# Optimization experiments

Measured on AMD Instinct MI355X. Metric: run time of the kernel, lower is better.

## Reference

```python
import jax, jax.numpy as jnp
import numpy as np

B, S, FC, FO = 16, 512, 24, 16
D, H, DK, FF, L = 512, 8, 64, 2048, 4
MAXPOS = 512
EPS = 1e-6


def _ln(x, scale, bias):
    mu = jnp.mean(x, axis=-1, keepdims=True)
    var = jnp.mean((x - mu) ** 2, axis=-1, keepdims=True)
    return (x - mu) * jax.lax.rsqrt(var + EPS) * scale + bias


def setup_inputs() -> dict:
    key = jax.random.key(0)
    ks = iter(jax.random.split(key, 64))
    def rn(shape, s=0.02):
        return (jax.random.normal(next(ks), shape, dtype=jnp.float32) * s)
    inp = {
        'x_cgm': jax.random.normal(next(ks), (B, S, FC), dtype=jnp.float32),
        'x_other': jax.random.normal(next(ks), (B, FO), dtype=jnp.float32),
        'cgm_W': rn((FC, D)), 'cgm_b': jnp.zeros((D,), jnp.float32),
        'rel_emb': rn((2 * MAXPOS - 1, DK)),
        'Wq': rn((L, D, H * DK)), 'bq': jnp.zeros((L, H * DK), jnp.float32),
        'Wk': rn((L, D, H * DK)), 'bk': jnp.zeros((L, H * DK), jnp.float32),
        'Wv': rn((L, D, H * DK)), 'bv': jnp.zeros((L, H * DK), jnp.float32),
        'Wo': rn((L, H * DK, D)), 'bo': jnp.zeros((L, D), jnp.float32),
        'Wg': rn((L, D, D)), 'bg': jnp.zeros((L, D), jnp.float32),
        'Wf1': rn((L, D, FF)), 'bf1': jnp.zeros((L, FF), jnp.float32),
        'Wfg': rn((L, D, FF)), 'bfg': jnp.zeros((L, FF), jnp.float32),
        'Wf2': rn((L, FF, D)), 'bf2': jnp.zeros((L, D), jnp.float32),
        'ln1_s': jnp.ones((L, D), jnp.float32), 'ln1_b': jnp.zeros((L, D), jnp.float32),
        'ln2_s': jnp.ones((L, D), jnp.float32), 'ln2_b': jnp.zeros((L, D), jnp.float32),
        'other_W': rn((FO, D)), 'other_b': jnp.zeros((D,), jnp.float32),
        'fW1': rn((2 * D, 256)), 'fb1': jnp.zeros((256,), jnp.float32),
        'fln1_s': jnp.ones((256,), jnp.float32), 'fln1_b': jnp.zeros((256,), jnp.float32),
        'fW2': rn((256, 128)), 'fb2': jnp.zeros((128,), jnp.float32),
        'fln2_s': jnp.ones((128,), jnp.float32), 'fln2_b': jnp.zeros((128,), jnp.float32),
        'fW3': rn((128, 1)), 'fb3': jnp.zeros((1,), jnp.float32),
    }
    return inp


def reference(x_cgm, x_other, cgm_W, cgm_b, rel_emb, Wq, bq, Wk, bk, Wv, bv,
              Wo, bo, Wg, bg, Wf1, bf1, Wfg, bfg, Wf2, bf2,
              ln1_s, ln1_b, ln2_s, ln2_b, other_W, other_b,
              fW1, fb1, fln1_s, fln1_b, fW2, fb2, fln2_s, fln2_b, fW3, fb3):
    x = x_cgm @ cgm_W + cgm_b  # [B,S,D]
    # relative position bias: rel_emb[i-j+MAXPOS-1] -> [S,S,DK], reduced by mean over depth
    idx = jnp.arange(S)
    pos_idx = idx[:, None] - idx[None, :] + MAXPOS - 1
    pos_bias = jnp.mean(rel_emb[pos_idx], axis=-1)  # [S,S]
    scale = jnp.sqrt(jnp.float32(DK))
    for l in range(L):
        q = (x @ Wq[l] + bq[l]).reshape(B, S, H, DK)
        k = (x @ Wk[l] + bk[l]).reshape(B, S, H, DK)
        v = (x @ Wv[l] + bv[l]).reshape(B, S, H, DK)
        scores = jnp.einsum('bqhd,bkhd->bhqk', q, k) / scale + pos_bias  # [B,H,S,S]
        probs = jax.nn.softmax(scores, axis=-1)
        ctx = jnp.einsum('bhqk,bkhd->bqhd', probs, v).reshape(B, S, H * DK)
        att = ctx @ Wo[l] + bo[l]
        gate = jax.nn.sigmoid(x @ Wg[l] + bg[l])
        x = _ln(x + gate * att, ln1_s[l], ln1_b[l])
        ff = (x @ Wf1[l] + bf1[l]) * jax.nn.sigmoid(x @ Wfg[l] + bfg[l])
        ff = ff @ Wf2[l] + bf2[l]
        x = _ln(x + ff, ln2_s[l], ln2_b[l])
    x = jnp.mean(x, axis=1)  # [B,D]
    xo = x_other @ other_W + other_b
    h = jnp.concatenate([x, xo], axis=-1)  # [B,2D]
    h = jax.nn.relu(_ln(h @ fW1 + fb1, fln1_s, fln1_b))
    h = jax.nn.relu(_ln(h @ fW2 + fb2, fln2_s, fln2_b))
    return h @ fW3 + fb3  # [B,1]
```

## Files before the change

kernel.cpp:

```cpp
#include <hip/hip_runtime.h>
#include <math.h>

constexpr int Bn = 16;
constexpr int Sn = 512;
constexpr int FCn = 24;
constexpr int FOn = 16;
constexpr int Dn = 512;
constexpr int Hn = 8;
constexpr int DKn = 64;
constexpr int FFn = 2048;
constexpr int Ln = 4;
constexpr int MAXPOSn = 512;
constexpr float EPSf = 1e-6f;

typedef __attribute__((ext_vector_type(8))) short bf16x8;
typedef __attribute__((ext_vector_type(4))) float floatx4;

__device__ __forceinline__ float sigmoidf_(float x) { return 1.0f / (1.0f + __expf(-x)); }

__device__ __forceinline__ unsigned short f2bf(float f) {
  unsigned int u = __float_as_uint(f);
  u += 0x7fffu + ((u >> 16) & 1u);
  return (unsigned short)(u >> 16);
}
__device__ __forceinline__ float b2f(unsigned short b) {
  return __uint_as_float(((unsigned int)b) << 16);
}

__device__ __forceinline__ void g2l16(const void* g, void* l) {
  __builtin_amdgcn_global_load_lds((const __attribute__((address_space(1))) void*)g,
                                   (__attribute__((address_space(3))) void*)l, 16, 0, 0);
}

__device__ __forceinline__ void st_bf16_pair(unsigned short* dst, float v, int lane) {
  unsigned int us = f2bf(v);
  unsigned int other = (unsigned int)__shfl_xor((int)us, 1);
  if (!(lane & 1)) *(unsigned int*)dst = us | (other << 16);
}

__device__ __forceinline__ float waveReduceSum(float v) {
  #pragma unroll
  for (int off = 32; off >= 1; off >>= 1) v += __shfl_xor(v, off);
  return v;
}

__device__ __forceinline__ float blockReduceSum(float v) {
  v = waveReduceSum(v);
  __shared__ float red[8];
  const int w = threadIdx.x >> 6;
  const int nw = blockDim.x >> 6;
  if ((threadIdx.x & 63) == 0) red[w] = v;
  __syncthreads();
  float r = 0.0f;
  for (int i = 0; i < nw; ++i) r += red[i];
  __syncthreads();
  return r;
}

__global__ __launch_bounds__(256) void wconv_kernel(
    const float* __restrict__ in, unsigned short* __restrict__ out,
    int K, int N, size_t inStride, size_t outStride) {
  __shared__ float tile[32][33];
  in += (size_t)blockIdx.z * inStride;
  out += (size_t)blockIdx.z * outStride;
  const int k0 = blockIdx.y * 32, n0 = blockIdx.x * 32;
  const int tr = threadIdx.x >> 3;
  const int tc4 = (threadIdx.x & 7) * 4;
  float4 vv = *(const float4*)&in[(size_t)(k0 + tr) * N + n0 + tc4];
  tile[tr][tc4 + 0] = vv.x; tile[tr][tc4 + 1] = vv.y;
  tile[tr][tc4 + 2] = vv.z; tile[tr][tc4 + 3] = vv.w;
  __syncthreads();
  ushort4 o4;
  o4.x = f2bf(tile[tc4 + 0][tr]); o4.y = f2bf(tile[tc4 + 1][tr]);
  o4.z = f2bf(tile[tc4 + 2][tr]); o4.w = f2bf(tile[tc4 + 3][tr]);
  *(ushort4*)&out[(size_t)(n0 + tr) * K + k0 + tc4] = o4;
}

__global__ void bcat_kernel(const float* __restrict__ bq, const float* __restrict__ bk,
                            const float* __restrict__ bv, const float* __restrict__ bg,
                            float* __restrict__ out) {
  const int t = blockIdx.x * 256 + threadIdx.x;
  const int l = t >> 11;
  const int c = t & 2047;
  float v;
  if (c < 512) v = bq[l * 512 + c];
  else if (c < 1024) v = bk[l * 512 + c - 512];
  else if (c < 1536) v = bv[l * 512 + c - 1024];
  else v = bg[l * 512 + c - 1536];
  out[t] = v;
}

__global__ __launch_bounds__(256) void embed_kernel(
    const float* __restrict__ xc, const float* __restrict__ W,
    const float* __restrict__ bias, float* __restrict__ x,
    unsigned short* __restrict__ xb) {
  const int idx = blockIdx.x * 256 + threadIdx.x;
  const int n = idx & (Dn - 1);
  const int m = idx >> 9;
  const float* xr = xc + m * FCn;
  float acc = bias[n];
  #pragma unroll
  for (int k = 0; k < FCn; ++k) acc = fmaf(xr[k], W[k * Dn + n], acc);
  x[idx] = acc;
  xb[idx] = f2bf(acc);
}

__global__ void relmean_kernel(const float* __restrict__ rel, float* __restrict__ rm) {
  const int p = blockIdx.x * blockDim.x + threadIdx.x;
  if (p >= 2 * MAXPOSn - 1) return;
  float s = 0.0f;
  #pragma unroll 8
  for (int d = 0; d < DKn; ++d) s += rel[p * DKn + d];
  rm[p] = s * (1.0f / DKn);
}

template <int EPI>
__global__ __launch_bounds__(256) void mgemm(
    const unsigned short* __restrict__ A, const unsigned short* __restrict__ Bt,
    const float* __restrict__ bias, float* __restrict__ Cf,
    unsigned short* __restrict__ Cb, unsigned short* __restrict__ Cb2,
    int Astride, int N, int Koff, int Klen, int ldc, int nt) {
  __shared__ unsigned short As[128 * 64];
  __shared__ unsigned short Bs[128 * 64];
  const int t = threadIdx.x;
  const int w = t >> 6;
  const int lane = t & 63;
  const int id = blockIdx.x;
  const int xcd = id & 7;
  const int lid = id >> 3;
  const int n0 = (lid % nt) * 128;
  const int m0 = (xcd * 8 + lid / nt) * 128;
  const int wm = (w >> 1) * 64;
  const int wn = (w & 1) * 64;
  const int lr = lane & 15;
  const int lq = lane >> 4;

  floatx4 acc[4][4];
  #pragma unroll
  for (int i = 0; i < 4; ++i)
    #pragma unroll
    for (int j = 0; j < 4; ++j) acc[i][j] = (floatx4){0.f, 0.f, 0.f, 0.f};

  const int srow = lane >> 3;
  const int sg = ((lane & 7) ^ srow) * 8;
  const int r7 = lr & 7;
  const int p0 = (lq ^ r7) * 8;
  const int p1 = ((4 + lq) ^ r7) * 8;

  for (int k0 = Koff; k0 < Koff + Klen; k0 += 64) {
    __syncthreads();
    #pragma unroll
    for (int r = 0; r < 4; ++r) {
      const int rb = (w * 4 + r) * 8;
      g2l16(&A[(size_t)(m0 + rb + srow) * Astride + k0 + sg], &As[rb * 64]);
      g2l16(&Bt[(size_t)(n0 + rb + srow) * Astride + k0 + sg], &Bs[rb * 64]);
    }
    __syncthreads();
    #pragma unroll
    for (int s = 0; s < 2; ++s) {
      const int ps = s ? p1 : p0;
      bf16x8 af[4], bf[4];
      #pragma unroll
      for (int i = 0; i < 4; ++i)
        af[i] = *(const bf16x8*)&As[(wm + i * 16 + lr) * 64 + ps];
      #pragma unroll
      for (int j = 0; j < 4; ++j)
        bf[j] = *(const bf16x8*)&Bs[(wn + j * 16 + lr) * 64 + ps];
      #pragma unroll
      for (int i = 0; i < 4; ++i)
        #pragma unroll
        for (int j = 0; j < 4; ++j)
          acc[i][j] = __builtin_amdgcn_mfma_f32_16x16x32_bf16(af[i], bf[j], acc[i][j], 0, 0, 0);
    }
  }

  #pragma unroll
  for (int i = 0; i < 4; ++i) {
    const int row = m0 + wm + i * 16 + lq * 4;
    #pragma unroll
    for (int j = 0; j < 4; ++j) {
      const int col = n0 + wn + j * 16 + lr;
      const int colp = col & ~1;
      #pragma unroll
      for (int r = 0; r < 4; ++r) {
        if (EPI == 0) {
          Cf[(size_t)(row + r) * ldc + col] = acc[i][j][r] + bias[col];
        } else if (EPI == 5) {
          const size_t idx = (size_t)(row + r) * ldc + col;
          Cf[idx] += acc[i][j][r];
        } else if (EPI == 3) {
          st_bf16_pair(&Cb[(size_t)(row + r) * ldc + colp], acc[i][j][r] + bias[col], lane);
        } else if (EPI == 4) {
          const float va = acc[i][j][r] + bias[col];
          if (col < 1536)
            st_bf16_pair(&Cb[(size_t)(row + r) * 1536 + colp], va, lane);
          else
            st_bf16_pair(&Cb2[(size_t)(row + r) * 512 + (colp - 1536)], sigmoidf_(va), lane);
        }
      }
    }
  }
}

__global__ __launch_bounds__(256) void ffgemm(
    const unsigned short* __restrict__ A, const unsigned short* __restrict__ B1t,
    const unsigned short* __restrict__ B2t, const float* __restrict__ b1,
    const float* __restrict__ b2, unsigned short* __restrict__ C, int K) {
  __shared__ unsigned short As[128 * 64];
  __shared__ unsigned short B1s[64 * 64];
  __shared__ unsigned short B2s[64 * 64];
  const int t = threadIdx.x;
  const int w = t >> 6;
  const int lane = t & 63;
  const int id = blockIdx.x;
  const int xcd = id & 7;
  const int lid = id >> 3;
  const int n0 = (lid & 31) * 64;
  const int m0 = (xcd * 8 + (lid >> 5)) * 128;
  const int wm = (w >> 1) * 64;
  const int wn = (w & 1) * 32;
  const int lr = lane & 15;
  const int lq = lane >> 4;

  floatx4 a1[4][2], a2[4][2];
  #pragma unroll
  for (int i = 0; i < 4; ++i)
    #pragma unroll
    for (int j = 0; j < 2; ++j) {
      a1[i][j] = (floatx4){0.f, 0.f, 0.f, 0.f};
      a2[i][j] = (floatx4){0.f, 0.f, 0.f, 0.f};
    }

  const int srow = lane >> 3;
  const int sg = ((lane & 7) ^ srow) * 8;
  const int r7 = lr & 7;
  const int p0 = (lq ^ r7) * 8;
  const int p1 = ((4 + lq) ^ r7) * 8;

  for (int k0 = 0; k0 < K; k0 += 64) {
    __syncthreads();
    #pragma unroll
    for (int r = 0; r < 4; ++r) {
      const int rb = (w * 4 + r) * 8;
      g2l16(&A[(size_t)(m0 + rb + srow) * K + k0 + sg], &As[rb * 64]);
    }
    #pragma unroll
    for (int r = 0; r < 2; ++r) {
      const int rb = (w * 2 + r) * 8;
      g2l16(&B1t[(size_t)(n0 + rb + srow) * K + k0 + sg], &B1s[rb * 64]);
      g2l16(&B2t[(size_t)(n0 + rb + srow) * K + k0 + sg], &B2s[rb * 64]);
    }
    __syncthreads();
    #pragma unroll
    for (int s = 0; s < 2; ++s) {
      const int ps = s ? p1 : p0;
      bf16x8 af[4], f1[2], f2[2];
      #pragma unroll
      for (int i = 0; i < 4; ++i)
        af[i] = *(const bf16x8*)&As[(wm + i * 16 + lr) * 64 + ps];
      #pragma unroll
      for (int j = 0; j < 2; ++j) {
        f1[j] = *(const bf16x8*)&B1s[(wn + j * 16 + lr) * 64 + ps];
        f2[j] = *(const bf16x8*)&B2s[(wn + j * 16 + lr) * 64 + ps];
      }
      #pragma unroll
      for (int i = 0; i < 4; ++i)
        #pragma unroll
        for (int j = 0; j < 2; ++j) {
          a1[i][j] = __builtin_amdgcn_mfma_f32_16x16x32_bf16(af[i], f1[j], a1[i][j], 0, 0, 0);
          a2[i][j] = __builtin_amdgcn_mfma_f32_16x16x32_bf16(af[i], f2[j], a2[i][j], 0, 0, 0);
        }
    }
  }

  #pragma unroll
  for (int i = 0; i < 4; ++i) {
    const int row = m0 + wm + i * 16 + lq * 4;
    #pragma unroll
    for (int j = 0; j < 2; ++j) {
      const int col = n0 + wn + j * 16 + lr;
      const int colp = col & ~1;
      const float bb1 = b1[col], bb2 = b2[col];
      #pragma unroll
      for (int r = 0; r < 4; ++r) {
        const float f = (a1[i][j][r] + bb1) * sigmoidf_(a2[i][j][r] + bb2);
        st_bf16_pair(&C[(size_t)(row + r) * 2048 + colp], f, lane);
      }
    }
  }
}

__global__ __launch_bounds__(256) void attn_kernel(
    const unsigned short* __restrict__ qkv, const float* __restrict__ rm,
    unsigned short* __restrict__ ctx) {
  __shared__ unsigned short Ks[64 * 72];
  __shared__ unsigned short Vt[64 * 72];
  __shared__ unsigned short Pw[4][16 * 72];
  __shared__ float rml[576];
  const int t = threadIdx.x;
  const int w = t >> 6;
  const int lane = t & 63;
  const int lr = lane & 15;
  const int lq = lane >> 4;
  const int bid = blockIdx.x;
  const int b = bid & 15;
  const int h = (bid >> 4) & 7;
  const int qt = bid >> 7;
  const int q0 = qt * 64;
  const size_t rowb = (size_t)b * Sn * 1536;

  for (int i = t; i < 576; i += 256) rml[i] = rm[q0 + i];

  bf16x8 aq0, aq1;
  {
    const unsigned short* qp = &qkv[rowb + (size_t)(q0 + w * 16 + lr) * 1536 + h * 64 + lq * 8];
    aq0 = *(const bf16x8*)qp;
    aq1 = *(const bf16x8*)(qp + 32);
  }

  floatx4 o_acc[4];
  #pragma unroll
  for (int i = 0; i < 4; ++i) o_acc[i] = (floatx4){0.f, 0.f, 0.f, 0.f};
  float m_old[4] = {-1e30f, -1e30f, -1e30f, -1e30f};
  float l_sum[4] = {0.f, 0.f, 0.f, 0.f};

  const int skey = t >> 2;
  const int schk = (t & 3) * 16;
  const int vkp = t >> 4;
  const int vd4 = (t & 15) * 4;

  for (int kc = 0; kc < 8; ++kc) {
    __syncthreads();
    {
      const unsigned short* gk = &qkv[rowb + (size_t)(kc * 64 + skey) * 1536 + 512 + h * 64 + schk];
      *(bf16x8*)&Ks[skey * 72 + schk] = *(const bf16x8*)gk;
      *(bf16x8*)&Ks[skey * 72 + schk + 8] = *(const bf16x8*)(gk + 8);
    }
    #pragma unroll
    for (int pass = 0; pass < 2; ++pass) {
      const int kp = vkp + pass * 16;
      const unsigned short* gv = &qkv[rowb + (size_t)(kc * 64 + kp * 2) * 1536 + 1024 + h * 64 + vd4];
      ushort4 v0 = *(const ushort4*)gv;
      ushort4 v1 = *(const ushort4*)(gv + 1536);
      *(ushort2*)&Vt[(vd4 + 0) * 72 + kp * 2] = make_ushort2(v0.x, v1.x);
      *(ushort2*)&Vt[(vd4 + 1) * 72 + kp * 2] = make_ushort2(v0.y, v1.y);
      *(ushort2*)&Vt[(vd4 + 2) * 72 + kp * 2] = make_ushort2(v0.z, v1.z);
      *(ushort2*)&Vt[(vd4 + 3) * 72 + kp * 2] = make_ushort2(v0.w, v1.w);
    }
    __syncthreads();

    floatx4 s_acc[4];
    #pragma unroll
    for (int j = 0; j < 4; ++j) {
      bf16x8 b0 = *(const bf16x8*)&Ks[(j * 16 + lr) * 72 + lq * 8];
      bf16x8 b1 = *(const bf16x8*)&Ks[(j * 16 + lr) * 72 + 32 + lq * 8];
      s_acc[j] = __builtin_amdgcn_mfma_f32_16x16x32_bf16(aq0, b0, (floatx4){0.f, 0.f, 0.f, 0.f}, 0, 0, 0);
      s_acc[j] = __builtin_amdgcn_mfma_f32_16x16x32_bf16(aq1, b1, s_acc[j], 0, 0, 0);
    }

    float mloc[4] = {-1e30f, -1e30f, -1e30f, -1e30f};
    #pragma unroll
    for (int j = 0; j < 4; ++j) {
      const int key = kc * 64 + j * 16 + lr;
      #pragma unroll
      for (int r = 0; r < 4; ++r) {
        const float sv = s_acc[j][r] * 0.125f + rml[(w * 16 + lq * 4 + r) + 511 - key];
        s_acc[j][r] = sv;
        mloc[r] = fmaxf(mloc[r], sv);
      }
    }
    #pragma unroll
    for (int off = 1; off <= 8; off <<= 1)
      #pragma unroll
      for (int r = 0; r < 4; ++r) mloc[r] = fmaxf(mloc[r], __shfl_xor(mloc[r], off));

    float alpha[4], rsum[4];
    #pragma unroll
    for (int r = 0; r < 4; ++r) {
      const float mnew = fmaxf(m_old[r], mloc[r]);
      alpha[r] = __expf(m_old[r] - mnew);
      m_old[r] = mnew;
      rsum[r] = 0.f;
    }
    #pragma unroll
    for (int j = 0; j < 4; ++j)
      #pragma unroll
      for (int r = 0; r < 4; ++r) {
        const float p = __expf(s_acc[j][r] - m_old[r]);
        rsum[r] += p;
        Pw[w][(lq * 4 + r) * 72 + j * 16 + lr] = f2bf(p);
      }
    #pragma unroll
    for (int off = 1; off <= 8; off <<= 1)
      #pragma unroll
      for (int r = 0; r < 4; ++r) rsum[r] += __shfl_xor(rsum[r], off);
    #pragma unroll
    for (int r = 0; r < 4; ++r) l_sum[r] = l_sum[r] * alpha[r] + rsum[r];
    #pragma unroll
    for (int i = 0; i < 4; ++i)
      #pragma unroll
      for (int r = 0; r < 4; ++r) o_acc[i][r] *= alpha[r];

    bf16x8 ap0 = *(const bf16x8*)&Pw[w][lr * 72 + lq * 8];
    bf16x8 ap1 = *(const bf16x8*)&Pw[w][lr * 72 + 32 + lq * 8];
    #pragma unroll
    for (int i = 0; i < 4; ++i) {
      bf16x8 v0 = *(const bf16x8*)&Vt[(i * 16 + lr) * 72 + lq * 8];
      bf16x8 v1 = *(const bf16x8*)&Vt[(i * 16 + lr) * 72 + 32 + lq * 8];
      o_acc[i] = __builtin_amdgcn_mfma_f32_16x16x32_bf16(ap0, v0, o_acc[i], 0, 0, 0);
      o_acc[i] = __builtin_amdgcn_mfma_f32_16x16x32_bf16(ap1, v1, o_acc[i], 0, 0, 0);
    }
  }

  float rinv[4];
  #pragma unroll
  for (int r = 0; r < 4; ++r) rinv[r] = 1.0f / l_sum[r];
  #pragma unroll
  for (int i = 0; i < 4; ++i)
    #pragma unroll
    for (int r = 0; r < 4; ++r) {
      const int q = q0 + w * 16 + lq * 4 + r;
      ctx[((size_t)(b * Sn + q)) * Dn + h * 64 + i * 16 + lr] = f2bf(o_acc[i][r] * rinv[r]);
    }
}

__global__ __launch_bounds__(256) void ln_res1_kernel(
    float* __restrict__ x, unsigned short* __restrict__ xb,
    const unsigned short* __restrict__ att, const unsigned short* __restrict__ gate,
    const float* __restrict__ s, const float* __restrict__ bsh) {
  const int w = threadIdx.x >> 6, lane = threadIdx.x & 63;
  const int row = blockIdx.x * 4 + w;
  const size_t base = (size_t)row * Dn;
  const int c = lane * 4;
  float4 xv0 = *(const float4*)&x[base + c];
  float4 xv1 = *(const float4*)&x[base + c + 256];
  ushort4 a0 = *(const ushort4*)&att[base + c];
  ushort4 a1 = *(const ushort4*)&att[base + c + 256];
  ushort4 g0 = *(const ushort4*)&gate[base + c];
  ushort4 g1 = *(const ushort4*)&gate[base + c + 256];
  float y[8];
  y[0] = xv0.x + b2f(a0.x) * b2f(g0.x);
  y[1] = xv0.y + b2f(a0.y) * b2f(g0.y);
  y[2] = xv0.z + b2f(a0.z) * b2f(g0.z);
  y[3] = xv0.w + b2f(a0.w) * b2f(g0.w);
  y[4] = xv1.x + b2f(a1.x) * b2f(g1.x);
  y[5] = xv1.y + b2f(a1.y) * b2f(g1.y);
  y[6] = xv1.z + b2f(a1.z) * b2f(g1.z);
  y[7] = xv1.w + b2f(a1.w) * b2f(g1.w);
  float sum = 0.f;
  #pragma unroll
  for (int i = 0; i < 8; ++i) sum += y[i];
  const float mu = waveReduceSum(sum) * (1.0f / Dn);
  float vs = 0.f;
  #pragma unroll
  for (int i = 0; i < 8; ++i) { y[i] -= mu; vs += y[i] * y[i]; }
  const float rstd = rsqrtf(waveReduceSum(vs) * (1.0f / Dn) + EPSf);
  float4 s0 = *(const float4*)&s[c], s1 = *(const float4*)&s[c + 256];
  float4 b0 = *(const float4*)&bsh[c], b1 = *(const float4*)&bsh[c + 256];
  float4 o0, o1;
  o0.x = y[0] * rstd * s0.x + b0.x; o0.y = y[1] * rstd * s0.y + b0.y;
  o0.z = y[2] * rstd * s0.z + b0.z; o0.w = y[3] * rstd * s0.w + b0.w;
  o1.x = y[4] * rstd * s1.x + b1.x; o1.y = y[5] * rstd * s1.y + b1.y;
  o1.z = y[6] * rstd * s1.z + b1.z; o1.w = y[7] * rstd * s1.w + b1.w;
  *(float4*)&x[base + c] = o0;
  *(float4*)&x[base + c + 256] = o1;
  ushort4 ob0, ob1;
  ob0.x = f2bf(o0.x); ob0.y = f2bf(o0.y); ob0.z = f2bf(o0.z); ob0.w = f2bf(o0.w);
  ob1.x = f2bf(o1.x); ob1.y = f2bf(o1.y); ob1.z = f2bf(o1.z); ob1.w = f2bf(o1.w);
  *(ushort4*)&xb[base + c] = ob0;
  *(ushort4*)&xb[base + c + 256] = ob1;
}

__global__ __launch_bounds__(256) void ln_res2_kernel(
    float* __restrict__ x, unsigned short* __restrict__ xb,
    const float* __restrict__ add, const float* __restrict__ s,
    const float* __restrict__ bsh) {
  const int w = threadIdx.x >> 6, lane = threadIdx.x & 63;
  const int row = blockIdx.x * 4 + w;
  const size_t base = (size_t)row * Dn;
  const int c = lane * 4;
  float4 xv0 = *(const float4*)&x[base + c];
  float4 xv1 = *(const float4*)&x[base + c + 256];
  float4 a0 = *(const float4*)&add[base + c];
  float4 a1 = *(const float4*)&add[base + c + 256];
  float y[8] = {xv0.x + a0.x, xv0.y + a0.y, xv0.z + a0.z, xv0.w + a0.w,
                xv1.x + a1.x, xv1.y + a1.y, xv1.z + a1.z, xv1.w + a1.w};
  float sum = 0.f;
  #pragma unroll
  for (int i = 0; i < 8; ++i) sum += y[i];
  const float mu = waveReduceSum(sum) * (1.0f / Dn);
  float vs = 0.f;
  #pragma unroll
  for (int i = 0; i < 8; ++i) { y[i] -= mu; vs += y[i] * y[i]; }
  const float rstd = rsqrtf(waveReduceSum(vs) * (1.0f / Dn) + EPSf);
  float4 s0 = *(const float4*)&s[c], s1 = *(const float4*)&s[c + 256];
  float4 b0 = *(const float4*)&bsh[c], b1 = *(const float4*)&bsh[c + 256];
  float4 o0, o1;
  o0.x = y[0] * rstd * s0.x + b0.x; o0.y = y[1] * rstd * s0.y + b0.y;
  o0.z = y[2] * rstd * s0.z + b0.z; o0.w = y[3] * rstd * s0.w + b0.w;
  o1.x = y[4] * rstd * s1.x + b1.x; o1.y = y[5] * rstd * s1.y + b1.y;
  o1.z = y[6] * rstd * s1.z + b1.z; o1.w = y[7] * rstd * s1.w + b1.w;
  *(float4*)&x[base + c] = o0;
  *(float4*)&x[base + c + 256] = o1;
  ushort4 ob0, ob1;
  ob0.x = f2bf(o0.x); ob0.y = f2bf(o0.y); ob0.z = f2bf(o0.z); ob0.w = f2bf(o0.w);
  ob1.x = f2bf(o1.x); ob1.y = f2bf(o1.y); ob1.z = f2bf(o1.z); ob1.w = f2bf(o1.w);
  *(ushort4*)&xb[base + c] = ob0;
  *(ushort4*)&xb[base + c + 256] = ob1;
}

__global__ __launch_bounds__(256) void mp_part_kernel(const float* __restrict__ x,
                                                      float* __restrict__ part) {
  const int b = blockIdx.x, sc = blockIdx.y;
  const int t = threadIdx.x;
  float s0 = 0.f, s1 = 0.f;
  for (int si = sc * 64; si < sc * 64 + 64; ++si) {
    s0 += x[((size_t)(b * Sn + si)) * Dn + t];
    s1 += x[((size_t)(b * Sn + si)) * Dn + t + 256];
  }
  part[(size_t)(b * 8 + sc) * 512 + t] = s0;
  part[(size_t)(b * 8 + sc) * 512 + t + 256] = s1;
}

__global__ __launch_bounds__(256) void mp_comb_xo_kernel(
    const float* __restrict__ part, const float* __restrict__ xo,
    const float* __restrict__ oW, const float* __restrict__ ob,
    float* __restrict__ h) {
  const int idx = blockIdx.x * 256 + threadIdx.x;
  const int b = idx >> 9, d = idx & 511;
  float s = 0.f;
  #pragma unroll
  for (int i = 0; i < 8; ++i) s += part[(size_t)(b * 8 + i) * 512 + d];
  h[b * 1024 + d] = s * (1.0f / Sn);
  float acc = ob[d];
  #pragma unroll
  for (int k = 0; k < FOn; ++k) acc = fmaf(xo[b * FOn + k], oW[k * Dn + d], acc);
  h[b * 1024 + 512 + d] = acc;
}

__global__ __launch_bounds__(256) void f1a_kernel(
    const float* __restrict__ h, const float* __restrict__ W,
    float* __restrict__ part) {
  const int b = blockIdx.x, kq = blockIdx.y;
  const int n = threadIdx.x;
  const float* hr = h + b * 1024 + kq * 128;
  const float* Wp = W + (size_t)(kq * 128) * 256 + n;
  float acc = 0.f;
  #pragma unroll 8
  for (int k = 0; k < 128; ++k) acc = fmaf(hr[k], Wp[(size_t)k * 256], acc);
  part[(size_t)(b * 8 + kq) * 256 + n] = acc;
}

__global__ __launch_bounds__(256) void tail_kernel(
    const float* __restrict__ part, const float* __restrict__ fb1,
    const float* __restrict__ fln1_s, const float* __restrict__ fln1_b,
    const float* __restrict__ fW2, const float* __restrict__ fb2,
    const float* __restrict__ fln2_s, const float* __restrict__ fln2_b,
    const float* __restrict__ fW3, const float* __restrict__ fb3,
    float* __restrict__ out) {
  __shared__ float h1[256];
  const int b = blockIdx.x;
  const int t = threadIdx.x;
  float acc = fb1[t];
  #pragma unroll
  for (int i = 0; i < 8; ++i) acc += part[(size_t)(b * 8 + i) * 256 + t];
  float mu = blockReduceSum(acc) * (1.0f / 256.0f);
  float d = acc - mu;
  float var = blockReduceSum(d * d) * (1.0f / 256.0f);
  h1[t] = fmaxf(d * rsqrtf(var + EPSf) * fln1_s[t] + fln1_b[t], 0.0f);
  __syncthreads();
  float acc2 = 0.f;
  if (t < 128) {
    #pragma unroll 8
    for (int k = 0; k < 256; ++k) acc2 = fmaf(h1[k], fW2[k * 128 + t], acc2);
    acc2 += fb2[t];
  }
  mu = blockReduceSum(t < 128 ? acc2 : 0.f) * (1.0f / 128.0f);
  d = (t < 128) ? acc2 - mu : 0.f;
  var = blockReduceSum(d * d) * (1.0f / 128.0f);
  float v = 0.f;
  if (t < 128) {
    const float h2v = fmaxf(d * rsqrtf(var + EPSf) * fln2_s[t] + fln2_b[t], 0.0f);
    v = h2v * fW3[t];
  }
  v = blockReduceSum(v);
  if (t == 0) out[b] = v + fb3[0];
}

extern "C" void kernel_launch(void* const* d_in, const int* in_sizes, int n_in,
                              void* d_out, int out_size, void* d_ws, size_t ws_size,
                              hipStream_t stream) {
  (void)in_sizes; (void)n_in; (void)out_size; (void)ws_size;
  const float* x_cgm  = (const float*)d_in[0];
  const float* x_other= (const float*)d_in[1];
  const float* cgm_W  = (const float*)d_in[2];
  const float* cgm_b  = (const float*)d_in[3];
  const float* rel_emb= (const float*)d_in[4];
  const float* Wq = (const float*)d_in[5];
  const float* bq = (const float*)d_in[6];
  const float* Wk = (const float*)d_in[7];
  const float* bk = (const float*)d_in[8];
  const float* Wv = (const float*)d_in[9];
  const float* bv = (const float*)d_in[10];
  const float* Wo = (const float*)d_in[11];
  const float* bo = (const float*)d_in[12];
  const float* Wg = (const float*)d_in[13];
  const float* bg = (const float*)d_in[14];
  const float* Wf1 = (const float*)d_in[15];
  const float* bf1 = (const float*)d_in[16];
  const float* Wfg = (const float*)d_in[17];
  const float* bfg = (const float*)d_in[18];
  const float* Wf2 = (const float*)d_in[19];
  const float* bf2 = (const float*)d_in[20];
  const float* ln1_s = (const float*)d_in[21];
  const float* ln1_b = (const float*)d_in[22];
  const float* ln2_s = (const float*)d_in[23];
  const float* ln2_b = (const float*)d_in[24];
  const float* other_W = (const float*)d_in[25];
  const float* other_b = (const float*)d_in[26];
  const float* fW1 = (const float*)d_in[27];
  const float* fb1 = (const float*)d_in[28];
  const float* fln1_s = (const float*)d_in[29];
  const float* fln1_b = (const float*)d_in[30];
  const float* fW2 = (const float*)d_in[31];
  const float* fb2 = (const float*)d_in[32];
  const float* fln2_s = (const float*)d_in[33];
  const float* fln2_b = (const float*)d_in[34];
  const float* fW3 = (const float*)d_in[35];
  const float* fb3 = (const float*)d_in[36];
  float* out = (float*)d_out;

  char* p = (char*)d_ws;
  auto alloc = [&](size_t bytes) { char* r = p; p += (bytes + 255) & ~(size_t)255; return r; };
  float*          X      = (float*)alloc((size_t)8192 * 512 * 4);
  unsigned short* Xb     = (unsigned short*)alloc((size_t)8192 * 512 * 2);
  unsigned short* QKVb   = (unsigned short*)alloc((size_t)8192 * 1536 * 2);
  unsigned short* CTXb   = (unsigned short*)alloc((size_t)8192 * 512 * 2);
  char*           R      = alloc((size_t)8192 * 2048 * 2);
  unsigned short* ATTb   = (unsigned short*)R;
  unsigned short* GATEb  = (unsigned short*)(R + (size_t)8192 * 512 * 2);
  unsigned short* FFBh   = (unsigned short*)R;
  float*          CTXo   = (float*)QKVb;
  unsigned short* Wqkvgt = (unsigned short*)alloc((size_t)4 * 2048 * 512 * 2);
  unsigned short* Wot    = (unsigned short*)alloc((size_t)4 * 512 * 512 * 2);
  unsigned short* Wf1t   = (unsigned short*)alloc((size_t)4 * 2048 * 512 * 2);
  unsigned short* Wfgt   = (unsigned short*)alloc((size_t)4 * 2048 * 512 * 2);
  unsigned short* Wf2t   = (unsigned short*)alloc((size_t)4 * 512 * 2048 * 2);
  float*          bqkvg  = (float*)alloc((size_t)4 * 2048 * 4);
  float*          RMb    = (float*)alloc(1024 * 4);
  float*          Hb     = (float*)alloc(16 * 1024 * 4);
  float*          MPP    = (float*)alloc((size_t)16 * 8 * 512 * 4);
  float*          F1P    = (float*)alloc((size_t)16 * 8 * 256 * 4);

  wconv_kernel<<<dim3(16, 16, 4), 256, 0, stream>>>(Wq, Wqkvgt + (size_t)0 * 512, 512, 512,
                                                    (size_t)512 * 512, (size_t)2048 * 512);
  wconv_kernel<<<dim3(16, 16, 4), 256, 0, stream>>>(Wk, Wqkvgt + (size_t)512 * 512, 512, 512,
                                                    (size_t)512 * 512, (size_t)2048 * 512);
  wconv_kernel<<<dim3(16, 16, 4), 256, 0, stream>>>(Wv, Wqkvgt + (size_t)1024 * 512, 512, 512,
                                                    (size_t)512 * 512, (size_t)2048 * 512);
  wconv_kernel<<<dim3(16, 16, 4), 256, 0, stream>>>(Wg, Wqkvgt + (size_t)1536 * 512, 512, 512,
                                                    (size_t)512 * 512, (size_t)2048 * 512);
  wconv_kernel<<<dim3(16, 16, 4), 256, 0, stream>>>(Wo, Wot, 512, 512,
                                                    (size_t)512 * 512, (size_t)512 * 512);
  wconv_kernel<<<dim3(64, 16, 4), 256, 0, stream>>>(Wf1, Wf1t, 512, 2048,
                                                    (size_t)512 * 2048, (size_t)2048 * 512);
  wconv_kernel<<<dim3(64, 16, 4), 256, 0, stream>>>(Wfg, Wfgt, 512, 2048,
                                                    (size_t)512 * 2048, (size_t)2048 * 512);
  wconv_kernel<<<dim3(16, 64, 4), 256, 0, stream>>>(Wf2, Wf2t, 2048, 512,
                                                    (size_t)2048 * 512, (size_t)512 * 2048);
  bcat_kernel<<<dim3(32), 256, 0, stream>>>(bq, bk, bv, bg, bqkvg);

  embed_kernel<<<dim3(16384), dim3(256), 0, stream>>>(x_cgm, cgm_W, cgm_b, X, Xb);
  relmean_kernel<<<dim3(4), dim3(256), 0, stream>>>(rel_emb, RMb);

  for (int l = 0; l < Ln; ++l) {
    const size_t bof = (size_t)l * Dn;
    mgemm<4><<<dim3(1024), 256, 0, stream>>>(Xb, Wqkvgt + (size_t)l * 2048 * 512,
                                             bqkvg + (size_t)l * 2048, nullptr, QKVb, GATEb,
                                             512, 2048, 0, 512, 0, 16);
    attn_kernel<<<dim3(1024), dim3(256), 0, stream>>>(QKVb, RMb, CTXb);
    mgemm<3><<<dim3(256), 256, 0, stream>>>(CTXb, Wot + (size_t)l * 512 * 512,
                                            bo + bof, nullptr, ATTb, nullptr,
                                            512, 512, 0, 512, 512, 4);
    ln_res1_kernel<<<dim3(2048), 256, 0, stream>>>(X, Xb, ATTb, GATEb, ln1_s + bof, ln1_b + bof);
    ffgemm<<<dim3(2048), 256, 0, stream>>>(Xb, Wf1t + (size_t)l * 2048 * 512,
                                           Wfgt + (size_t)l * 2048 * 512,
                                           bf1 + (size_t)l * FFn, bfg + (size_t)l * FFn,
                                           FFBh, 512);
    mgemm<0><<<dim3(256), 256, 0, stream>>>(FFBh, Wf2t + (size_t)l * 512 * 2048,
                                            bf2 + bof, CTXo, nullptr, nullptr,
                                            2048, 512, 0, 1024, 512, 4);
    mgemm<5><<<dim3(256), 256, 0, stream>>>(FFBh, Wf2t + (size_t)l * 512 * 2048,
                                            nullptr, CTXo, nullptr, nullptr,
                                            2048, 512, 1024, 1024, 512, 4);
    ln_res2_kernel<<<dim3(2048), 256, 0, stream>>>(X, Xb, CTXo, ln2_s + bof, ln2_b + bof);
  }

  mp_part_kernel<<<dim3(16, 8), 256, 0, stream>>>(X, MPP);
  mp_comb_xo_kernel<<<dim3(32), 256, 0, stream>>>(MPP, x_other, other_W, other_b, Hb);
  f1a_kernel<<<dim3(16, 8), 256, 0, stream>>>(Hb, fW1, F1P);
  tail_kernel<<<dim3(16), 256, 0, stream>>>(F1P, fb1, fln1_s, fln1_b,
                                            fW2, fb2, fln2_s, fln2_b, fW3, fb3, out);
}
```

Baseline: 1.213 ms.

## Shrink GEMM K-tile to 32, add 128x64 GEMM for N=512, drop split-K

All bf16 MFMA GEMMs now stage K tiles of 32 instead of 64, with a plain unswizzled LDS layout and one MFMA step per tile. A new mgemm_n64 kernel with 128x64 output tiles handles the two N=512 GEMMs (output projection and FF down-projection) on 512 blocks instead of 256. The FF down-projection is no longer split into two K halves accumulated through a read-modify-write pass; one kernel covers the full K=2048. The aim is more parallelism, less LDS per block and one fewer launch, at the cost of twice as many barriers per K, possible LDS bank conflicts without the XOR swizzle, and less reuse per tile.

Result: faster. 1.101 ms (-9.2%).

```diff
diff --git a/kernel.cpp b/kernel.cpp
--- a/kernel.cpp
+++ b/kernel.cpp
@@ -119,9 +119,9 @@
     const unsigned short* __restrict__ A, const unsigned short* __restrict__ Bt,
     const float* __restrict__ bias, float* __restrict__ Cf,
     unsigned short* __restrict__ Cb, unsigned short* __restrict__ Cb2,
-    int Astride, int N, int Koff, int Klen, int ldc, int nt) {
-  __shared__ unsigned short As[128 * 64];
-  __shared__ unsigned short Bs[128 * 64];
+    int Astride, int N, int Klen, int ldc, int nt) {
+  __shared__ unsigned short As[128 * 32];
+  __shared__ unsigned short Bs[128 * 32];
   const int t = threadIdx.x;
   const int w = t >> 6;
   const int lane = t & 63;
@@ -141,37 +141,30 @@
     #pragma unroll
     for (int j = 0; j < 4; ++j) acc[i][j] = (floatx4){0.f, 0.f, 0.f, 0.f};
 
-  const int srow = lane >> 3;
-  const int sg = ((lane & 7) ^ srow) * 8;
-  const int r7 = lr & 7;
-  const int p0 = (lq ^ r7) * 8;
-  const int p1 = ((4 + lq) ^ r7) * 8;
-
-  for (int k0 = Koff; k0 < Koff + Klen; k0 += 64) {
+  const int srow = lane >> 2;
+  const int schk = (lane & 3) * 8;
+
+  for (int k0 = 0; k0 < Klen; k0 += 32) {
     __syncthreads();
     #pragma unroll
-    for (int r = 0; r < 4; ++r) {
-      const int rb = (w * 4 + r) * 8;
-      g2l16(&A[(size_t)(m0 + rb + srow) * Astride + k0 + sg], &As[rb * 64]);
-      g2l16(&Bt[(size_t)(n0 + rb + srow) * Astride + k0 + sg], &Bs[rb * 64]);
+    for (int r = 0; r < 2; ++r) {
+      const int rb = (w * 2 + r) * 16;
+      g2l16(&A[(size_t)(m0 + rb + srow) * Astride + k0 + schk], &As[rb * 32]);
+      g2l16(&Bt[(size_t)(n0 + rb + srow) * Astride + k0 + schk], &Bs[rb * 32]);
     }
     __syncthreads();
-    #pragma unroll
-    for (int s = 0; s < 2; ++s) {
-      const int ps = s ? p1 : p0;
-      bf16x8 af[4], bf[4];
-      #pragma unroll
-      for (int i = 0; i < 4; ++i)
-        af[i] = *(const bf16x8*)&As[(wm + i * 16 + lr) * 64 + ps];
+    bf16x8 af[4], bf[4];
+    #pragma unroll
+    for (int i = 0; i < 4; ++i)
+      af[i] = *(const bf16x8*)&As[(wm + i * 16 + lr) * 32 + lq * 8];
+    #pragma unroll
+    for (int j = 0; j < 4; ++j)
+      bf[j] = *(const bf16x8*)&Bs[(wn + j * 16 + lr) * 32 + lq * 8];
+    #pragma unroll
+    for (int i = 0; i < 4; ++i)
       #pragma unroll
       for (int j = 0; j < 4; ++j)
-        bf[j] = *(const bf16x8*)&Bs[(wn + j * 16 + lr) * 64 + ps];
-      #pragma unroll
-      for (int i = 0; i < 4; ++i)
-        #pragma unroll
-        for (int j = 0; j < 4; ++j)
-          acc[i][j] = __builtin_amdgcn_mfma_f32_16x16x32_bf16(af[i], bf[j], acc[i][j], 0, 0, 0);
-    }
+        acc[i][j] = __builtin_amdgcn_mfma_f32_16x16x32_bf16(af[i], bf[j], acc[i][j], 0, 0, 0);
   }
 
   #pragma unroll
@@ -185,9 +178,6 @@
       for (int r = 0; r < 4; ++r) {
         if (EPI == 0) {
           Cf[(size_t)(row + r) * ldc + col] = acc[i][j][r] + bias[col];
-        } else if (EPI == 5) {
-          const size_t idx = (size_t)(row + r) * ldc + col;
-          Cf[idx] += acc[i][j][r];
         } else if (EPI == 3) {
           st_bf16_pair(&Cb[(size_t)(row + r) * ldc + colp], acc[i][j][r] + bias[col], lane);
         } else if (EPI == 4) {
@@ -202,13 +192,85 @@
   }
 }
 
+template <int EPI>
+__global__ __launch_bounds__(256) void mgemm_n64(
+    const unsigned short* __restrict__ A, const unsigned short* __restrict__ Bt,
+    const float* __restrict__ bias, float* __restrict__ Cf,
+    unsigned short* __restrict__ Cb, int Astride, int Klen, int ldc) {
+  __shared__ unsigned short As[128 * 32];
+  __shared__ unsigned short Bs[64 * 32];
+  const int t = threadIdx.x;
+  const int w = t >> 6;
+  const int lane = t & 63;
+  const int id = blockIdx.x;
+  const int xcd = id & 7;
+  const int lid = id >> 3;
+  const int n0 = (lid & 7) * 64;
+  const int m0 = (xcd * 8 + (lid >> 3)) * 128;
+  const int wm = (w >> 1) * 64;
+  const int wn = (w & 1) * 32;
+  const int lr = lane & 15;
+  const int lq = lane >> 4;
+
+  floatx4 acc[4][2];
+  #pragma unroll
+  for (int i = 0; i < 4; ++i)
+    #pragma unroll
+    for (int j = 0; j < 2; ++j) acc[i][j] = (floatx4){0.f, 0.f, 0.f, 0.f};
+
+  const int srow = lane >> 2;
+  const int schk = (lane & 3) * 8;
+
+  for (int k0 = 0; k0 < Klen; k0 += 32) {
+    __syncthreads();
+    #pragma unroll
+    for (int r = 0; r < 2; ++r) {
+      const int rb = (w * 2 + r) * 16;
+      g2l16(&A[(size_t)(m0 + rb + srow) * Astride + k0 + schk], &As[rb * 32]);
+    }
+    g2l16(&Bt[(size_t)(n0 + w * 16 + srow) * Astride + k0 + schk], &Bs[(w * 16) * 32]);
+    __syncthreads();
+    bf16x8 af[4], bf[2];
+    #pragma unroll
+    for (int i = 0; i < 4; ++i)
+      af[i] = *(const bf16x8*)&As[(wm + i * 16 + lr) * 32 + lq * 8];
+    #pragma unroll
+    for (int j = 0; j < 2; ++j)
+      bf[j] = *(const bf16x8*)&Bs[(wn + j * 16 + lr) * 32 + lq * 8];
+    #pragma unroll
+    for (int i = 0; i < 4; ++i)
+      #pragma unroll
+      for (int j = 0; j < 2; ++j)
+        acc[i][j] = __builtin_amdgcn_mfma_f32_16x16x32_bf16(af[i], bf[j], acc[i][j], 0, 0, 0);
+  }
+
+  #pragma unroll
+  for (int i = 0; i < 4; ++i) {
+    const int row = m0 + wm + i * 16 + lq * 4;
+    #pragma unroll
+    for (int j = 0; j < 2; ++j) {
+      const int col = n0 + wn + j * 16 + lr;
+      const int colp = col & ~1;
+      const float bv = bias[col];
+      #pragma unroll
+      for (int r = 0; r < 4; ++r) {
+        if (EPI == 0) {
+          Cf[(size_t)(row + r) * ldc + col] = acc[i][j][r] + bv;
+        } else {
+          st_bf16_pair(&Cb[(size_t)(row + r) * ldc + colp], acc[i][j][r] + bv, lane);
+        }
+      }
+    }
+  }
+}
+
 __global__ __launch_bounds__(256) void ffgemm(
     const unsigned short* __restrict__ A, const unsigned short* __restrict__ B1t,
     const unsigned short* __restrict__ B2t, const float* __restrict__ b1,
     const float* __restrict__ b2, unsigned short* __restrict__ C, int K) {
-  __shared__ unsigned short As[128 * 64];
-  __shared__ unsigned short B1s[64 * 64];
-  __shared__ unsigned short B2s[64 * 64];
+  __shared__ unsigned short As[128 * 32];
+  __shared__ unsigned short B1s[64 * 32];
+  __shared__ unsigned short B2s[64 * 32];
   const int t = threadIdx.x;
   const int w = t >> 6;
   const int lane = t & 63;
@@ -231,46 +293,32 @@
       a2[i][j] = (floatx4){0.f, 0.f, 0.f, 0.f};
     }
 
-  const int srow = lane >> 3;
-  const int sg = ((lane & 7) ^ srow) * 8;
-  const int r7 = lr & 7;
-  const int p0 = (lq ^ r7) * 8;
-  const int p1 = ((4 + lq) ^ r7) * 8;
-
-  for (int k0 = 0; k0 < K; k0 += 64) {
+  const int srow = lane >> 2;
+  const int schk = (lane & 3) * 8;
+
+  for (int k0 = 0; k0 < K; k0 += 32) {
     __syncthreads();
-    #pragma unroll
-    for (int r = 0; r < 4; ++r) {
-      const int rb = (w * 4 + r) * 8;
-      g2l16(&A[(size_t)(m0 + rb + srow) * K + k0 + sg], &As[rb * 64]);
-    }
-    #pragma unroll
-    for (int r = 0; r < 2; ++r) {
-      const int rb = (w * 2 + r) * 8;
-      g2l16(&B1t[(size_t)(n0 + rb + srow) * K + k0 + sg], &B1s[rb * 64]);
-      g2l16(&B2t[(size_t)(n0 + rb + srow) * K + k0 + sg], &B2s[rb * 64]);
-    }
+    g2l16(&A[(size_t)(m0 + w * 32 + srow) * K + k0 + schk], &As[(w * 32) * 32]);
+    g2l16(&A[(size_t)(m0 + w * 32 + 16 + srow) * K + k0 + schk], &As[(w * 32 + 16) * 32]);
+    g2l16(&B1t[(size_t)(n0 + w * 16 + srow) * K + k0 + schk], &B1s[(w * 16) * 32]);
+    g2l16(&B2t[(size_t)(n0 + w * 16 + srow) * K + k0 + schk], &B2s[(w * 16) * 32]);
     __syncthreads();
-    #pragma unroll
-    for (int s = 0; s < 2; ++s) {
-      const int ps = s ? p1 : p0;
-      bf16x8 af[4], f1[2], f2[2];
-      #pragma unroll
-      for (int i = 0; i < 4; ++i)
-        af[i] = *(const bf16x8*)&As[(wm + i * 16 + lr) * 64 + ps];
+    bf16x8 af[4], f1[2], f2[2];
+    #pragma unroll
+    for (int i = 0; i < 4; ++i)
+      af[i] = *(const bf16x8*)&As[(wm + i * 16 + lr) * 32 + lq * 8];
+    #pragma unroll
+    for (int j = 0; j < 2; ++j) {
+      f1[j] = *(const bf16x8*)&B1s[(wn + j * 16 + lr) * 32 + lq * 8];
+      f2[j] = *(const bf16x8*)&B2s[(wn + j * 16 + lr) * 32 + lq * 8];
+    }
+    #pragma unroll
+    for (int i = 0; i < 4; ++i)
       #pragma unroll
       for (int j = 0; j < 2; ++j) {
-        f1[j] = *(const bf16x8*)&B1s[(wn + j * 16 + lr) * 64 + ps];
-        f2[j] = *(const bf16x8*)&B2s[(wn + j * 16 + lr) * 64 + ps];
+        a1[i][j] = __builtin_amdgcn_mfma_f32_16x16x32_bf16(af[i], f1[j], a1[i][j], 0, 0, 0);
+        a2[i][j] = __builtin_amdgcn_mfma_f32_16x16x32_bf16(af[i], f2[j], a2[i][j], 0, 0, 0);
       }
-      #pragma unroll
-      for (int i = 0; i < 4; ++i)
-        #pragma unroll
-        for (int j = 0; j < 2; ++j) {
-          a1[i][j] = __builtin_amdgcn_mfma_f32_16x16x32_bf16(af[i], f1[j], a1[i][j], 0, 0, 0);
-          a2[i][j] = __builtin_amdgcn_mfma_f32_16x16x32_bf16(af[i], f2[j], a2[i][j], 0, 0, 0);
-        }
-    }
   }
 
   #pragma unroll
@@ -677,22 +725,17 @@
     const size_t bof = (size_t)l * Dn;
     mgemm<4><<<dim3(1024), 256, 0, stream>>>(Xb, Wqkvgt + (size_t)l * 2048 * 512,
                                              bqkvg + (size_t)l * 2048, nullptr, QKVb, GATEb,
-                                             512, 2048, 0, 512, 0, 16);
+                                             512, 2048, 512, 0, 16);
     attn_kernel<<<dim3(1024), dim3(256), 0, stream>>>(QKVb, RMb, CTXb);
-    mgemm<3><<<dim3(256), 256, 0, stream>>>(CTXb, Wot + (size_t)l * 512 * 512,
-                                            bo + bof, nullptr, ATTb, nullptr,
-                                            512, 512, 0, 512, 512, 4);
+    mgemm_n64<3><<<dim3(512), 256, 0, stream>>>(CTXb, Wot + (size_t)l * 512 * 512,
+                                                bo + bof, nullptr, ATTb, 512, 512, 512);
     ln_res1_kernel<<<dim3(2048), 256, 0, stream>>>(X, Xb, ATTb, GATEb, ln1_s + bof, ln1_b + bof);
     ffgemm<<<dim3(2048), 256, 0, stream>>>(Xb, Wf1t + (size_t)l * 2048 * 512,
                                            Wfgt + (size_t)l * 2048 * 512,
                                            bf1 + (size_t)l * FFn, bfg + (size_t)l * FFn,
                                            FFBh, 512);
-    mgemm<0><<<dim3(256), 256, 0, stream>>>(FFBh, Wf2t + (size_t)l * 512 * 2048,
-                                            bf2 + bof, CTXo, nullptr, nullptr,
-                                            2048, 512, 0, 1024, 512, 4);
-    mgemm<5><<<dim3(256), 256, 0, stream>>>(FFBh, Wf2t + (size_t)l * 512 * 2048,
-                                            nullptr, CTXo, nullptr, nullptr,
-                                            2048, 512, 1024, 1024, 512, 4);
+    mgemm_n64<0><<<dim3(512), 256, 0, stream>>>(FFBh, Wf2t + (size_t)l * 512 * 2048,
+                                                bf2 + bof, CTXo, nullptr, 2048, 2048, 512);
     ln_res2_kernel<<<dim3(2048), 256, 0, stream>>>(X, Xb, CTXo, ln2_s + bof, ln2_b + bof);
   }
 
```
